# Performance work log

Measured on AMD Instinct MI355X. Metric: run time of the kernel, lower is better.

## Reference

```python
import jax, jax.numpy as jnp
import numpy as np

SEQ, BATCH, IN_DIM, HID = 1024, 512, 128, 128


def _linear_params(key, fan_in, fan_out):
    # matches torch nn.Linear default init: U(-1/sqrt(fan_in), 1/sqrt(fan_in))
    s = 1.0 / np.sqrt(fan_in)
    k1, k2 = jax.random.split(key)
    W = jax.random.uniform(k1, (fan_in, fan_out), minval=-s, maxval=s, dtype=jnp.float32)
    b = jax.random.uniform(k2, (fan_out,), minval=-s, maxval=s, dtype=jnp.float32)
    return W, b


def setup_inputs() -> dict:
    key = jax.random.key(0)
    ks = jax.random.split(key, 5)
    inputs = jax.random.normal(ks[0], (SEQ, BATCH, IN_DIM), dtype=jnp.float32)
    Wf, bf = _linear_params(ks[1], IN_DIM + HID, HID)
    Wi, bi = _linear_params(ks[2], IN_DIM + HID, HID)
    Wg, bg = _linear_params(ks[3], IN_DIM + HID, HID)
    Wo, bo = _linear_params(ks[4], IN_DIM + HID, HID)
    return {"inputs": inputs, "Wf": Wf, "bf": bf, "Wi": Wi, "bi": bi,
            "Wg": Wg, "bg": bg, "Wo": Wo, "bo": bo}


def reference(inputs, Wf, bf, Wi, bi, Wg, bg, Wo, bo):
    # inputs: [seq, batch, in_dim] (time-major, matches torch unbind(dim=0))
    B = inputs.shape[1]
    H = Wf.shape[1]
    h0 = jnp.zeros((B, H), dtype=inputs.dtype)
    c0 = jnp.zeros((B, H), dtype=inputs.dtype)

    def step(carry, x):
        hx, cx = carry
        comb = jnp.concatenate([x, hx], axis=1)  # [B, in_dim+H]
        f_lin = comb @ Wf + bf
        i_lin = comb @ Wi + bi
        g = jnp.tanh(comb @ Wg + bg)
        o = jax.nn.sigmoid(comb @ Wo + bo)
        # Quantum sampler, closed form:
        #  - RX(theta)|0> has <Z> = cos(theta)
        #  - CNOT chain over f-wires pulls Z_j back to Z_0...Z_j -> cumprod of cos
        #  - i-wires untouched by CNOTs -> plain cos
        #  probs = (<Z> + 1) / 2
        f = (jnp.cumprod(jnp.cos(f_lin), axis=1) + 1.0) * 0.5
        i = (jnp.cos(i_lin) + 1.0) * 0.5
        cx_new = f * cx + i * g
        hx_new = o * jnp.tanh(cx_new)
        return (hx_new, cx_new), hx_new

    (hx, cx), outputs = jax.lax.scan(step, (h0, c0), inputs)
    return outputs, hx, cx
```

## Files before the change

### kernel.cpp

```cpp
#include <hip/hip_runtime.h>

#define SEQ   1024
#define BATCH 512
#define HID   128

typedef __attribute__((ext_vector_type(8))) short          short8v;
typedef __attribute__((ext_vector_type(4))) float          float4v;
typedef __attribute__((ext_vector_type(4))) unsigned short ushort4v;

__device__ __forceinline__ unsigned short f2bf(float f) {
    union { float f; unsigned u; } v; v.f = f;
    return (unsigned short)((v.u + 0x7fffu + ((v.u >> 16) & 1u)) >> 16);
}
__device__ __forceinline__ float bf2f(unsigned short u) {
    union { unsigned u; float f; } v; v.u = ((unsigned)u) << 16;
    return v.f;
}
__device__ __forceinline__ unsigned packbf(float a, float b) {
    return (unsigned)f2bf(a) | ((unsigned)f2bf(b) << 16);
}
__device__ __forceinline__ float fast_cos(float x) {
    return __builtin_amdgcn_cosf(x * 0.15915494309189535f);
}
__device__ __forceinline__ float fast_sigmoid(float x) {
    return __builtin_amdgcn_rcpf(1.0f + __builtin_amdgcn_exp2f(-1.4426950408889634f * x));
}
__device__ __forceinline__ float fast_tanh(float x) {
    return 1.0f - 2.0f * __builtin_amdgcn_rcpf(1.0f + __builtin_amdgcn_exp2f(2.8853900817779268f * x));
}
template<int CTRL, int RM>
__device__ __forceinline__ float dpp1(float v) {
    union { float f; int i; } s, o, r;
    s.f = v; o.f = 1.0f;
    r.i = __builtin_amdgcn_update_dpp(o.i, s.i, CTRL, RM, 0xf, false);
    return r.f;
}
#define BAR() do { asm volatile("s_waitcnt lgkmcnt(0)" ::: "memory");  \
                   __builtin_amdgcn_s_barrier();                       \
                   __builtin_amdgcn_sched_barrier(0); } while (0)

__device__ __forceinline__ int zswz(int slot, int g, int c) {
    return slot * 512 + g * 128 + (c ^ ((c >> 5) << 4) ^ ((slot & 2) << 3));
}
__device__ __forceinline__ int gswz(int row, int g, int c) {
    return row * 512 + g * 128 + (c ^ ((c >> 5) << 4));
}

__global__ __launch_bounds__(512, 1) void qlstm_fused(
    const float* __restrict__ X,
    const float* __restrict__ Wf, const float* __restrict__ bfp,
    const float* __restrict__ Wi, const float* __restrict__ bip,
    const float* __restrict__ Wg, const float* __restrict__ bgp,
    const float* __restrict__ Wo, const float* __restrict__ bop,
    float* __restrict__ out)
{
    __shared__ short8v  wx_lds[8][4][4][64];
    __shared__ unsigned zr_lds[8 * 4 * 128];
    __shared__ float    ga_lds[2 * 4 * 128];
    __shared__ alignas(8)  unsigned short h_bf[2][HID];
    __shared__ alignas(16) unsigned short x_win[2][8][HID];
    __shared__ float scanT[2];

    const int tid = threadIdx.x, lane = tid & 63, wid = tid >> 6;
    const int l15 = lane & 15, kg = lane >> 4;
    const int b0 = blockIdx.x * 2;
    const int g  = wid >> 1;
    const int hb = wid & 1;
    const int cb = hb * 64;
    const float* Wsel = (g == 0) ? Wf : (g == 1) ? Wi : (g == 2) ? Wg : Wo;
    const float* bsel = (g == 0) ? bfp : (g == 1) ? bip : (g == 2) ? bgp : bop;

    #pragma unroll
    for (int n = 0; n < 4; ++n) {
        const int col = cb + n * 16 + l15;
        #pragma unroll
        for (int ks = 0; ks < 4; ++ks) {
            short8v wx;
            #pragma unroll
            for (int j = 0; j < 8; ++j)
                wx[j] = (short)f2bf(Wsel[(size_t)(ks * 32 + kg * 8 + j) * HID + col]);
            wx_lds[wid][n][ks][lane] = wx;
        }
    }
    BAR();

    short8v bwh[4][4];
    #pragma unroll
    for (int n = 0; n < 4; ++n) {
        const int col = cb + n * 16 + l15;
        #pragma unroll
        for (int ks = 0; ks < 4; ++ks) {
            short8v wh;
            #pragma unroll
            for (int j = 0; j < 8; ++j)
                wh[j] = (short)f2bf(Wsel[(size_t)(128 + ks * 32 + kg * 8 + j) * HID + col]);
            bwh[n][ks] = wh;
        }
    }
    float biasr[4];
    #pragma unroll
    for (int n = 0; n < 4; ++n) biasr[n] = bsel[cb + n * 16 + l15];

    if (tid < 128) ((unsigned*)h_bf)[tid] = 0u;

    const int crow = wid >> 1;
    const int ccol = (wid & 1) * 64 + lane;
    float c_reg = 0.f, h_last = 0.f;
    const int c_act = cb + lane;

    const int pt = tid - 256;
    const int sm = (pt >> 5) & 7;
    const int sc = pt & 31;
    const size_t xrow_off = ((size_t)(b0 + (sm & 1))) * HID + sc * 4;
    const int xw_boff = sm * 256 + ((((sc >> 1) ^ (sm & 7)) << 4) | ((sc & 1) << 3));

#define STAGE_XWIN(buf, s0) do {                                                    \
    const float* xp_ = X + ((size_t)((s0) + (sm >> 1)) * BATCH) * HID + xrow_off;   \
    float4v a_ = *(const float4v*)xp_;                                              \
    ushort4v o_;                                                                    \
    o_[0] = f2bf(a_[0]); o_[1] = f2bf(a_[1]); o_[2] = f2bf(a_[2]); o_[3] = f2bf(a_[3]); \
    *(ushort4v*)((char*)&x_win[buf][0][0] + xw_boff) = o_;                          \
} while (0)

#define XTILE(i, bn, buf) do {                                                      \
    float4v xa_;                                                                    \
    xa_[0] = biasr[i]; xa_[1] = biasr[i]; xa_[2] = biasr[i]; xa_[3] = biasr[i];     \
    _Pragma("unroll")                                                               \
    for (int ks_ = 0; ks_ < 4; ++ks_) {                                             \
        short8v axk = *(const short8v*)((const char*)&x_win[buf][0][0] +            \
            ((l15 & 7) * 256 + (((ks_ * 4 + kg) ^ (l15 & 7)) << 4)));               \
        xa_ = __builtin_amdgcn_mfma_f32_16x16x32_bf16(axk, wx_lds[wid][i][ks_][lane], xa_, 0, 0, 0); \
    }                                                                               \
    if (kg < 2) {                                                                   \
        const int cs_ = cb + (i) * 16 + l15;                                        \
        zr_lds[zswz(((bn) + kg * 2) & 7,     g, cs_)] = packbf(xa_[0], xa_[1]);     \
        zr_lds[zswz(((bn) + kg * 2 + 1) & 7, g, cs_)] = packbf(xa_[2], xa_[3]);     \
    }                                                                               \
} while (0)

    if (wid >= 4) { STAGE_XWIN(0, 0); STAGE_XWIN(1, 4); }
    BAR();
    XTILE(0, 0, 0);
    XTILE(1, 0, 0);
    XTILE(2, 0, 0);
    XTILE(3, 0, 0);
    BAR();

    float4v xg = {};

    #pragma unroll 1
    for (int t = 0; t < SEQ; ++t) {
        const int w = t & 3;
        const int W = t >> 2;
        const int bnext = (t & ~3) + 4;

        const unsigned zp = zr_lds[zswz(t & 7, g, c_act)];
        short8v ah[4];
        #pragma unroll
        for (int ks = 0; ks < 4; ++ks)
            ah[ks] = *(const short8v*)&h_bf[l15 & 1][ks * 32 + kg * 8];

        if (w == 0 && wid >= 4 && bnext + 4 < SEQ) {
            xg = *(const float4v*)(X + ((size_t)(bnext + 4 + (sm >> 1)) * BATCH) * HID + xrow_off);
        }

        float4v acc[4];
        #pragma unroll
        for (int n = 0; n < 4; ++n)
            #pragma unroll
            for (int j = 0; j < 4; ++j) acc[n][j] = 0.f;
        __builtin_amdgcn_s_setprio(1);
        #pragma unroll
        for (int ks = 0; ks < 4; ++ks)
            #pragma unroll
            for (int n = 0; n < 4; ++n)
                acc[n] = __builtin_amdgcn_mfma_f32_16x16x32_bf16(ah[ks], bwh[n][ks], acc[n], 0, 0, 0);
        __builtin_amdgcn_s_setprio(0);

        if (bnext < SEQ) {
            const int xbuf = (W + 1) & 1;
            switch (w) {
                case 0: XTILE(0, bnext, xbuf); break;
                case 1: XTILE(1, bnext, xbuf); break;
                case 2: XTILE(2, bnext, xbuf); break;
                default: XTILE(3, bnext, xbuf); break;
            }
        }

        float s0 = ((kg == 0) ? acc[0][0] : (kg == 1) ? acc[1][0]
                  : (kg == 2) ? acc[2][0] : acc[3][0]) + bf2f((unsigned short)(zp & 0xffffu));
        float s1 = ((kg == 0) ? acc[0][1] : (kg == 1) ? acc[1][1]
                  : (kg == 2) ? acc[2][1] : acc[3][1]) + bf2f((unsigned short)(zp >> 16));

        float v0, v1;
        if (g == 0) {
            float S0 = fast_cos(s0), S1 = fast_cos(s1);
            S0 *= dpp1<0x111, 0xf>(S0);  S1 *= dpp1<0x111, 0xf>(S1);
            S0 *= dpp1<0x112, 0xf>(S0);  S1 *= dpp1<0x112, 0xf>(S1);
            S0 *= dpp1<0x114, 0xf>(S0);  S1 *= dpp1<0x114, 0xf>(S1);
            S0 *= dpp1<0x118, 0xf>(S0);  S1 *= dpp1<0x118, 0xf>(S1);
            const float T00 = __shfl(S0, 15), T01 = __shfl(S0, 31), T02 = __shfl(S0, 47);
            const float T10 = __shfl(S1, 15), T11 = __shfl(S1, 31), T12 = __shfl(S1, 47);
            const float rp0 = (kg == 0) ? 1.f : (kg == 1) ? T00
                            : (kg == 2) ? T00 * T01 : T00 * T01 * T02;
            const float rp1 = (kg == 0) ? 1.f : (kg == 1) ? T10
                            : (kg == 2) ? T10 * T11 : T10 * T11 * T12;
            v0 = rp0 * S0;
            v1 = rp1 * S1;
            if (wid == 0 && lane == 63) { scanT[0] = v0; scanT[1] = v1; }
        } else if (g == 1) {
            v0 = (fast_cos(s0) + 1.f) * .5f;
            v1 = (fast_cos(s1) + 1.f) * .5f;
        } else if (g == 2) {
            v0 = fast_tanh(s0);
            v1 = fast_tanh(s1);
        } else {
            v0 = fast_sigmoid(s0);
            v1 = fast_sigmoid(s1);
        }
        ga_lds[gswz(0, g, c_act)] = v0;
        ga_lds[gswz(1, g, c_act)] = v1;

        BAR();

        if (wid < 4) {
            float fv = ga_lds[gswz(crow, 0, ccol)];
            if (wid & 1) fv *= scanT[crow];
            const float f  = (fv + 1.f) * 0.5f;
            const float iv = ga_lds[gswz(crow, 1, ccol)];
            const float gv = ga_lds[gswz(crow, 2, ccol)];
            const float ov = ga_lds[gswz(crow, 3, ccol)];
            const float cn = fmaf(f, c_reg, iv * gv);
            const float hn = ov * fast_tanh(cn);
            c_reg = cn; h_last = hn;
            h_bf[crow][ccol] = f2bf(hn);
            out[((size_t)t * BATCH + b0 + crow) * HID + ccol] = hn;
        } else if (w == 2 && bnext + 4 < SEQ) {
            ushort4v o_;
            o_[0] = f2bf(xg[0]); o_[1] = f2bf(xg[1]); o_[2] = f2bf(xg[2]); o_[3] = f2bf(xg[3]);
            *(ushort4v*)((char*)&x_win[W & 1][0][0] + xw_boff) = o_;
        }
        BAR();
    }

    if (wid < 4) {
        const size_t base = (size_t)SEQ * BATCH * HID;
        const size_t ro = (size_t)(b0 + crow) * HID + ccol;
        out[base + ro] = h_last;
        out[base + (size_t)BATCH * HID + ro] = c_reg;
    }
#undef STAGE_XWIN
#undef XTILE
}

extern "C" void kernel_launch(void* const* d_in, const int* in_sizes, int n_in,
                              void* d_out, int out_size, void* d_ws, size_t ws_size,
                              hipStream_t stream) {
    const float* X  = (const float*)d_in[0];
    const float* Wf = (const float*)d_in[1];
    const float* bf = (const float*)d_in[2];
    const float* Wi = (const float*)d_in[3];
    const float* bi = (const float*)d_in[4];
    const float* Wg = (const float*)d_in[5];
    const float* bg = (const float*)d_in[6];
    const float* Wo = (const float*)d_in[7];
    const float* bo = (const float*)d_in[8];
    float* out = (float*)d_out;
    (void)d_ws; (void)ws_size;

    qlstm_fused<<<BATCH / 2, 512, 0, stream>>>(
        X, Wf, bf, Wi, bi, Wg, bg, Wo, bo, out);
}
```

Baseline: 1.105 ms.

## Assign all four gates per column to each wave, removing gate-exchange LDS round trip

```diff
diff --git a/kernel.cpp b/kernel.cpp
--- a/kernel.cpp
+++ b/kernel.cpp
@@ -41,9 +41,6 @@
 
 __device__ __forceinline__ int zswz(int slot, int g, int c) {
     return slot * 512 + g * 128 + (c ^ ((c >> 5) << 4) ^ ((slot & 2) << 3));
-}
-__device__ __forceinline__ int gswz(int row, int g, int c) {
-    return row * 512 + g * 128 + (c ^ ((c >> 5) << 4));
 }
 
 __global__ __launch_bounds__(512, 1) void qlstm_fused(
@@ -56,57 +53,49 @@
 {
     __shared__ short8v  wx_lds[8][4][4][64];
     __shared__ unsigned zr_lds[8 * 4 * 128];
-    __shared__ float    ga_lds[2 * 4 * 128];
     __shared__ alignas(8)  unsigned short h_bf[2][HID];
     __shared__ alignas(16) unsigned short x_win[2][8][HID];
-    __shared__ float scanT[2];
+    __shared__ float scanW[8][2];
 
     const int tid = threadIdx.x, lane = tid & 63, wid = tid >> 6;
     const int l15 = lane & 15, kg = lane >> 4;
     const int b0 = blockIdx.x * 2;
-    const int g  = wid >> 1;
-    const int hb = wid & 1;
-    const int cb = hb * 64;
-    const float* Wsel = (g == 0) ? Wf : (g == 1) ? Wi : (g == 2) ? Wg : Wo;
-    const float* bsel = (g == 0) ? bfp : (g == 1) ? bip : (g == 2) ? bgp : bop;
+    const int col = wid * 16 + l15;
 
     #pragma unroll
-    for (int n = 0; n < 4; ++n) {
-        const int col = cb + n * 16 + l15;
+    for (int g2 = 0; g2 < 4; ++g2) {
+        const float* Wsel = (g2 == 0) ? Wf : (g2 == 1) ? Wi : (g2 == 2) ? Wg : Wo;
         #pragma unroll
         for (int ks = 0; ks < 4; ++ks) {
             short8v wx;
             #pragma unroll
             for (int j = 0; j < 8; ++j)
                 wx[j] = (short)f2bf(Wsel[(size_t)(ks * 32 + kg * 8 + j) * HID + col]);
-            wx_lds[wid][n][ks][lane] = wx;
+            wx_lds[wid][g2][ks][lane] = wx;
         }
     }
     BAR();
 
     short8v bwh[4][4];
+    float biasr[4];
     #pragma unroll
-    for (int n = 0; n < 4; ++n) {
-        const int col = cb + n * 16 + l15;
+    for (int g2 = 0; g2 < 4; ++g2) {
+        const float* Wsel = (g2 == 0) ? Wf : (g2 == 1) ? Wi : (g2 == 2) ? Wg : Wo;
+        const float* bsel = (g2 == 0) ? bfp : (g2 == 1) ? bip : (g2 == 2) ? bgp : bop;
         #pragma unroll
         for (int ks = 0; ks < 4; ++ks) {
             short8v wh;
             #pragma unroll
             for (int j = 0; j < 8; ++j)
                 wh[j] = (short)f2bf(Wsel[(size_t)(128 + ks * 32 + kg * 8 + j) * HID + col]);
-            bwh[n][ks] = wh;
-        }
-    }
-    float biasr[4];
-    #pragma unroll
-    for (int n = 0; n < 4; ++n) biasr[n] = bsel[cb + n * 16 + l15];
+            bwh[g2][ks] = wh;
+        }
+        biasr[g2] = bsel[col];
+    }
 
     if (tid < 128) ((unsigned*)h_bf)[tid] = 0u;
 
-    const int crow = wid >> 1;
-    const int ccol = (wid & 1) * 64 + lane;
-    float c_reg = 0.f, h_last = 0.f;
-    const int c_act = cb + lane;
+    float c_r0 = 0.f, c_r1 = 0.f, hL0 = 0.f, hL1 = 0.f;
 
     const int pt = tid - 256;
     const int sm = (pt >> 5) & 7;
@@ -122,19 +111,18 @@
     *(ushort4v*)((char*)&x_win[buf][0][0] + xw_boff) = o_;                          \
 } while (0)
 
-#define XTILE(i, bn, buf) do {                                                      \
+#define XTILE(G, bn, buf) do {                                                      \
     float4v xa_;                                                                    \
-    xa_[0] = biasr[i]; xa_[1] = biasr[i]; xa_[2] = biasr[i]; xa_[3] = biasr[i];     \
+    xa_[0] = biasr[G]; xa_[1] = biasr[G]; xa_[2] = biasr[G]; xa_[3] = biasr[G];     \
     _Pragma("unroll")                                                               \
     for (int ks_ = 0; ks_ < 4; ++ks_) {                                             \
         short8v axk = *(const short8v*)((const char*)&x_win[buf][0][0] +            \
             ((l15 & 7) * 256 + (((ks_ * 4 + kg) ^ (l15 & 7)) << 4)));               \
-        xa_ = __builtin_amdgcn_mfma_f32_16x16x32_bf16(axk, wx_lds[wid][i][ks_][lane], xa_, 0, 0, 0); \
+        xa_ = __builtin_amdgcn_mfma_f32_16x16x32_bf16(axk, wx_lds[wid][G][ks_][lane], xa_, 0, 0, 0); \
     }                                                                               \
     if (kg < 2) {                                                                   \
-        const int cs_ = cb + (i) * 16 + l15;                                        \
-        zr_lds[zswz(((bn) + kg * 2) & 7,     g, cs_)] = packbf(xa_[0], xa_[1]);     \
-        zr_lds[zswz(((bn) + kg * 2 + 1) & 7, g, cs_)] = packbf(xa_[2], xa_[3]);     \
+        zr_lds[zswz(((bn) + kg * 2) & 7,     G, col)] = packbf(xa_[0], xa_[1]);     \
+        zr_lds[zswz(((bn) + kg * 2 + 1) & 7, G, col)] = packbf(xa_[2], xa_[3]);     \
     }                                                                               \
 } while (0)
 
@@ -154,27 +142,29 @@
         const int W = t >> 2;
         const int bnext = (t & ~3) + 4;
 
-        const unsigned zp = zr_lds[zswz(t & 7, g, c_act)];
+        unsigned zp[4];
+        #pragma unroll
+        for (int g2 = 0; g2 < 4; ++g2)
+            zp[g2] = zr_lds[zswz(t & 7, g2, col)];
         short8v ah[4];
         #pragma unroll
         for (int ks = 0; ks < 4; ++ks)
             ah[ks] = *(const short8v*)&h_bf[l15 & 1][ks * 32 + kg * 8];
 
-        if (w == 0 && wid >= 4 && bnext + 4 < SEQ) {
+        if (w == 0 && wid >= 4 && bnext + 4 < SEQ)
             xg = *(const float4v*)(X + ((size_t)(bnext + 4 + (sm >> 1)) * BATCH) * HID + xrow_off);
-        }
 
         float4v acc[4];
         #pragma unroll
-        for (int n = 0; n < 4; ++n)
-            #pragma unroll
-            for (int j = 0; j < 4; ++j) acc[n][j] = 0.f;
+        for (int g2 = 0; g2 < 4; ++g2)
+            #pragma unroll
+            for (int j = 0; j < 4; ++j) acc[g2][j] = 0.f;
         __builtin_amdgcn_s_setprio(1);
         #pragma unroll
-        for (int ks = 0; ks < 4; ++ks)
-            #pragma unroll
-            for (int n = 0; n < 4; ++n)
-                acc[n] = __builtin_amdgcn_mfma_f32_16x16x32_bf16(ah[ks], bwh[n][ks], acc[n], 0, 0, 0);
+        for (int g2 = 0; g2 < 4; ++g2)
+            #pragma unroll
+            for (int ks = 0; ks < 4; ++ks)
+                acc[g2] = __builtin_amdgcn_mfma_f32_16x16x32_bf16(ah[ks], bwh[g2][ks], acc[g2], 0, 0, 0);
         __builtin_amdgcn_s_setprio(0);
 
         if (bnext < SEQ) {
@@ -187,55 +177,47 @@
             }
         }
 
-        float s0 = ((kg == 0) ? acc[0][0] : (kg == 1) ? acc[1][0]
-                  : (kg == 2) ? acc[2][0] : acc[3][0]) + bf2f((unsigned short)(zp & 0xffffu));
-        float s1 = ((kg == 0) ? acc[0][1] : (kg == 1) ? acc[1][1]
-                  : (kg == 2) ? acc[2][1] : acc[3][1]) + bf2f((unsigned short)(zp >> 16));
-
-        float v0, v1;
-        if (g == 0) {
-            float S0 = fast_cos(s0), S1 = fast_cos(s1);
-            S0 *= dpp1<0x111, 0xf>(S0);  S1 *= dpp1<0x111, 0xf>(S1);
-            S0 *= dpp1<0x112, 0xf>(S0);  S1 *= dpp1<0x112, 0xf>(S1);
-            S0 *= dpp1<0x114, 0xf>(S0);  S1 *= dpp1<0x114, 0xf>(S1);
-            S0 *= dpp1<0x118, 0xf>(S0);  S1 *= dpp1<0x118, 0xf>(S1);
-            const float T00 = __shfl(S0, 15), T01 = __shfl(S0, 31), T02 = __shfl(S0, 47);
-            const float T10 = __shfl(S1, 15), T11 = __shfl(S1, 31), T12 = __shfl(S1, 47);
-            const float rp0 = (kg == 0) ? 1.f : (kg == 1) ? T00
-                            : (kg == 2) ? T00 * T01 : T00 * T01 * T02;
-            const float rp1 = (kg == 0) ? 1.f : (kg == 1) ? T10
-                            : (kg == 2) ? T10 * T11 : T10 * T11 * T12;
-            v0 = rp0 * S0;
-            v1 = rp1 * S1;
-            if (wid == 0 && lane == 63) { scanT[0] = v0; scanT[1] = v1; }
-        } else if (g == 1) {
-            v0 = (fast_cos(s0) + 1.f) * .5f;
-            v1 = (fast_cos(s1) + 1.f) * .5f;
-        } else if (g == 2) {
-            v0 = fast_tanh(s0);
-            v1 = fast_tanh(s1);
-        } else {
-            v0 = fast_sigmoid(s0);
-            v1 = fast_sigmoid(s1);
-        }
-        ga_lds[gswz(0, g, c_act)] = v0;
-        ga_lds[gswz(1, g, c_act)] = v1;
+        const float fc0 = fast_cos(acc[0][0] + bf2f((unsigned short)(zp[0] & 0xffffu)));
+        const float fc1 = fast_cos(acc[0][1] + bf2f((unsigned short)(zp[0] >> 16)));
+        const float iv0 = (fast_cos(acc[1][0] + bf2f((unsigned short)(zp[1] & 0xffffu))) + 1.f) * 0.5f;
+        const float iv1 = (fast_cos(acc[1][1] + bf2f((unsigned short)(zp[1] >> 16))) + 1.f) * 0.5f;
+        const float gv0 = fast_tanh(acc[2][0] + bf2f((unsigned short)(zp[2] & 0xffffu)));
+        const float gv1 = fast_tanh(acc[2][1] + bf2f((unsigned short)(zp[2] >> 16)));
+        const float ov0 = fast_sigmoid(acc[3][0] + bf2f((unsigned short)(zp[3] & 0xffffu)));
+        const float ov1 = fast_sigmoid(acc[3][1] + bf2f((unsigned short)(zp[3] >> 16)));
+
+        float S0 = fc0, S1 = fc1;
+        S0 *= dpp1<0x111, 0xf>(S0);  S1 *= dpp1<0x111, 0xf>(S1);
+        S0 *= dpp1<0x112, 0xf>(S0);  S1 *= dpp1<0x112, 0xf>(S1);
+        S0 *= dpp1<0x114, 0xf>(S0);  S1 *= dpp1<0x114, 0xf>(S1);
+        S0 *= dpp1<0x118, 0xf>(S0);  S1 *= dpp1<0x118, 0xf>(S1);
+        if (lane == 15) { scanW[wid][0] = S0; scanW[wid][1] = S1; }
 
         BAR();
 
-        if (wid < 4) {
-            float fv = ga_lds[gswz(crow, 0, ccol)];
-            if (wid & 1) fv *= scanT[crow];
-            const float f  = (fv + 1.f) * 0.5f;
-            const float iv = ga_lds[gswz(crow, 1, ccol)];
-            const float gv = ga_lds[gswz(crow, 2, ccol)];
-            const float ov = ga_lds[gswz(crow, 3, ccol)];
-            const float cn = fmaf(f, c_reg, iv * gv);
-            const float hn = ov * fast_tanh(cn);
-            c_reg = cn; h_last = hn;
-            h_bf[crow][ccol] = f2bf(hn);
-            out[((size_t)t * BATCH + b0 + crow) * HID + ccol] = hn;
-        } else if (w == 2 && bnext + 4 < SEQ) {
+        float p0 = 1.f, p1 = 1.f;
+        #pragma unroll
+        for (int jw = 0; jw < 8; ++jw) {
+            const float a = scanW[jw][0], b = scanW[jw][1];
+            p0 *= (jw < wid) ? a : 1.f;
+            p1 *= (jw < wid) ? b : 1.f;
+        }
+        const float f0 = (p0 * S0 + 1.f) * 0.5f;
+        const float f1 = (p1 * S1 + 1.f) * 0.5f;
+
+        const float cn0 = fmaf(f0, c_r0, iv0 * gv0);
+        const float cn1 = fmaf(f1, c_r1, iv1 * gv1);
+        const float hn0 = ov0 * fast_tanh(cn0);
+        const float hn1 = ov1 * fast_tanh(cn1);
+        c_r0 = cn0; c_r1 = cn1; hL0 = hn0; hL1 = hn1;
+
+        if (kg == 0) {
+            h_bf[0][col] = f2bf(hn0);
+            h_bf[1][col] = f2bf(hn1);
+            out[((size_t)t * BATCH + b0) * HID + col] = hn0;
+            out[((size_t)t * BATCH + b0 + 1) * HID + col] = hn1;
+        }
+        if (wid >= 4 && w == 2 && bnext + 4 < SEQ) {
             ushort4v o_;
             o_[0] = f2bf(xg[0]); o_[1] = f2bf(xg[1]); o_[2] = f2bf(xg[2]); o_[3] = f2bf(xg[3]);
             *(ushort4v*)((char*)&x_win[W & 1][0][0] + xw_boff) = o_;
@@ -243,11 +225,12 @@
         BAR();
     }
 
-    if (wid < 4) {
+    if (kg == 0) {
         const size_t base = (size_t)SEQ * BATCH * HID;
-        const size_t ro = (size_t)(b0 + crow) * HID + ccol;
-        out[base + ro] = h_last;
-        out[base + (size_t)BATCH * HID + ro] = c_reg;
+        out[base + (size_t)b0 * HID + col]       = hL0;
+        out[base + (size_t)(b0 + 1) * HID + col] = hL1;
+        out[base + (size_t)BATCH * HID + (size_t)b0 * HID + col]       = c_r0;
+        out[base + (size_t)BATCH * HID + (size_t)(b0 + 1) * HID + col] = c_r1;
     }
 #undef STAGE_XWIN
 #undef XTILE
```

After: 1.227 ms. 1.11x slower.

## Move input-projection MFMAs to idle waves during elementwise phase

Applied to the files above, without the earlier changes.

```diff
diff --git a/kernel.cpp b/kernel.cpp
--- a/kernel.cpp
+++ b/kernel.cpp
@@ -57,6 +57,7 @@
     __shared__ short8v  wx_lds[8][4][4][64];
     __shared__ unsigned zr_lds[8 * 4 * 128];
     __shared__ float    ga_lds[2 * 4 * 128];
+    __shared__ float    bias_lds[4 * 128];
     __shared__ alignas(8)  unsigned short h_bf[2][HID];
     __shared__ alignas(16) unsigned short x_win[2][8][HID];
     __shared__ float scanT[2];
@@ -96,10 +97,8 @@
                 wh[j] = (short)f2bf(Wsel[(size_t)(128 + ks * 32 + kg * 8 + j) * HID + col]);
             bwh[n][ks] = wh;
         }
-    }
-    float biasr[4];
-    #pragma unroll
-    for (int n = 0; n < 4; ++n) biasr[n] = bsel[cb + n * 16 + l15];
+        if (kg == 0) bias_lds[g * 128 + col] = bsel[col];
+    }
 
     if (tid < 128) ((unsigned*)h_bf)[tid] = 0u;
 
@@ -122,28 +121,37 @@
     *(ushort4v*)((char*)&x_win[buf][0][0] + xw_boff) = o_;                          \
 } while (0)
 
-#define XTILE(i, bn, buf) do {                                                      \
-    float4v xa_;                                                                    \
-    xa_[0] = biasr[i]; xa_[1] = biasr[i]; xa_[2] = biasr[i]; xa_[3] = biasr[i];     \
+#define XT2(i, bn, buf) do {                                                        \
+    short8v axk[4];                                                                 \
     _Pragma("unroll")                                                               \
-    for (int ks_ = 0; ks_ < 4; ++ks_) {                                             \
-        short8v axk = *(const short8v*)((const char*)&x_win[buf][0][0] +            \
+    for (int ks_ = 0; ks_ < 4; ++ks_)                                               \
+        axk[ks_] = *(const short8v*)((const char*)&x_win[buf][0][0] +               \
             ((l15 & 7) * 256 + (((ks_ * 4 + kg) ^ (l15 & 7)) << 4)));               \
-        xa_ = __builtin_amdgcn_mfma_f32_16x16x32_bf16(axk, wx_lds[wid][i][ks_][lane], xa_, 0, 0, 0); \
-    }                                                                               \
-    if (kg < 2) {                                                                   \
-        const int cs_ = cb + (i) * 16 + l15;                                        \
-        zr_lds[zswz(((bn) + kg * 2) & 7,     g, cs_)] = packbf(xa_[0], xa_[1]);     \
-        zr_lds[zswz(((bn) + kg * 2 + 1) & 7, g, cs_)] = packbf(xa_[2], xa_[3]);     \
+    _Pragma("unroll")                                                               \
+    for (int uh_ = 0; uh_ < 2; ++uh_) {                                             \
+        const int u_  = (wid - 4) * 2 + uh_;                                        \
+        const int cs_ = uh_ * 64 + (i) * 16 + l15;                                  \
+        const float bb_ = bias_lds[(wid - 4) * 128 + cs_];                          \
+        float4v xa_; xa_[0] = bb_; xa_[1] = bb_; xa_[2] = bb_; xa_[3] = bb_;        \
+        _Pragma("unroll")                                                           \
+        for (int ks_ = 0; ks_ < 4; ++ks_)                                           \
+            xa_ = __builtin_amdgcn_mfma_f32_16x16x32_bf16(axk[ks_],                 \
+                      wx_lds[u_][i][ks_][lane], xa_, 0, 0, 0);                      \
+        if (kg < 2) {                                                               \
+            zr_lds[zswz(((bn) + kg * 2) & 7,     wid - 4, cs_)] = packbf(xa_[0], xa_[1]); \
+            zr_lds[zswz(((bn) + kg * 2 + 1) & 7, wid - 4, cs_)] = packbf(xa_[2], xa_[3]); \
+        }                                                                           \
     }                                                                               \
 } while (0)
 
     if (wid >= 4) { STAGE_XWIN(0, 0); STAGE_XWIN(1, 4); }
     BAR();
-    XTILE(0, 0, 0);
-    XTILE(1, 0, 0);
-    XTILE(2, 0, 0);
-    XTILE(3, 0, 0);
+    if (wid >= 4) {
+        XT2(0, 0, 0);
+        XT2(1, 0, 0);
+        XT2(2, 0, 0);
+        XT2(3, 0, 0);
+    }
     BAR();
 
     float4v xg = {};
@@ -160,9 +168,8 @@
         for (int ks = 0; ks < 4; ++ks)
             ah[ks] = *(const short8v*)&h_bf[l15 & 1][ks * 32 + kg * 8];
 
-        if (w == 0 && wid >= 4 && bnext + 4 < SEQ) {
+        if (w == 0 && wid >= 4 && bnext + 4 < SEQ)
             xg = *(const float4v*)(X + ((size_t)(bnext + 4 + (sm >> 1)) * BATCH) * HID + xrow_off);
-        }
 
         float4v acc[4];
         #pragma unroll
@@ -176,16 +183,6 @@
             for (int n = 0; n < 4; ++n)
                 acc[n] = __builtin_amdgcn_mfma_f32_16x16x32_bf16(ah[ks], bwh[n][ks], acc[n], 0, 0, 0);
         __builtin_amdgcn_s_setprio(0);
-
-        if (bnext < SEQ) {
-            const int xbuf = (W + 1) & 1;
-            switch (w) {
-                case 0: XTILE(0, bnext, xbuf); break;
-                case 1: XTILE(1, bnext, xbuf); break;
-                case 2: XTILE(2, bnext, xbuf); break;
-                default: XTILE(3, bnext, xbuf); break;
-            }
-        }
 
         float s0 = ((kg == 0) ? acc[0][0] : (kg == 1) ? acc[1][0]
                   : (kg == 2) ? acc[2][0] : acc[3][0]) + bf2f((unsigned short)(zp & 0xffffu));
@@ -235,10 +232,21 @@
             c_reg = cn; h_last = hn;
             h_bf[crow][ccol] = f2bf(hn);
             out[((size_t)t * BATCH + b0 + crow) * HID + ccol] = hn;
-        } else if (w == 2 && bnext + 4 < SEQ) {
-            ushort4v o_;
-            o_[0] = f2bf(xg[0]); o_[1] = f2bf(xg[1]); o_[2] = f2bf(xg[2]); o_[3] = f2bf(xg[3]);
-            *(ushort4v*)((char*)&x_win[W & 1][0][0] + xw_boff) = o_;
+        } else {
+            if (bnext < SEQ) {
+                const int xbuf = (W + 1) & 1;
+                switch (w) {
+                    case 0: XT2(0, bnext, xbuf); break;
+                    case 1: XT2(1, bnext, xbuf); break;
+                    case 2: XT2(2, bnext, xbuf); break;
+                    default: XT2(3, bnext, xbuf); break;
+                }
+            }
+            if (w == 2 && bnext + 4 < SEQ) {
+                ushort4v o_;
+                o_[0] = f2bf(xg[0]); o_[1] = f2bf(xg[1]); o_[2] = f2bf(xg[2]); o_[3] = f2bf(xg[3]);
+                *(ushort4v*)((char*)&x_win[W & 1][0][0] + xw_boff) = o_;
+            }
         }
         BAR();
     }
@@ -250,7 +258,7 @@
         out[base + (size_t)BATCH * HID + ro] = c_reg;
     }
 #undef STAGE_XWIN
-#undef XTILE
+#undef XT2
 }
 
 extern "C" void kernel_launch(void* const* d_in, const int* in_sizes, int n_in,
```

Measured after the change: 1.194 ms. 1.08x slower.

## Split block into recurrent and producer waves for input projection

Applied to the files above, without the earlier changes.

```diff
diff --git a/kernel.cpp b/kernel.cpp
--- a/kernel.cpp
+++ b/kernel.cpp
@@ -46,7 +46,7 @@
     return row * 512 + g * 128 + (c ^ ((c >> 5) << 4));
 }
 
-__global__ __launch_bounds__(512, 1) void qlstm_fused(
+__global__ __launch_bounds__(1024, 1) void qlstm_fused(
     const float* __restrict__ X,
     const float* __restrict__ Wf, const float* __restrict__ bfp,
     const float* __restrict__ Wi, const float* __restrict__ bip,
@@ -54,173 +54,172 @@
     const float* __restrict__ Wo, const float* __restrict__ bop,
     float* __restrict__ out)
 {
-    __shared__ short8v  wx_lds[8][4][4][64];
-    __shared__ unsigned zr_lds[8 * 4 * 128];
+    __shared__ unsigned zr_lds[16 * 4 * 128];
     __shared__ float    ga_lds[2 * 4 * 128];
     __shared__ alignas(8)  unsigned short h_bf[2][HID];
-    __shared__ alignas(16) unsigned short x_win[2][8][HID];
+    __shared__ alignas(16) unsigned short x_win[2][16][HID];
     __shared__ float scanT[2];
 
     const int tid = threadIdx.x, lane = tid & 63, wid = tid >> 6;
     const int l15 = lane & 15, kg = lane >> 4;
     const int b0 = blockIdx.x * 2;
-    const int g  = wid >> 1;
-    const int hb = wid & 1;
+    const bool prod = (wid >= 8);
+    const int rr = prod ? (wid - 8) : wid;
+    const int g  = rr >> 1;
+    const int hb = rr & 1;
     const int cb = hb * 64;
     const float* Wsel = (g == 0) ? Wf : (g == 1) ? Wi : (g == 2) ? Wg : Wo;
     const float* bsel = (g == 0) ? bfp : (g == 1) ? bip : (g == 2) ? bgp : bop;
 
-    #pragma unroll
-    for (int n = 0; n < 4; ++n) {
-        const int col = cb + n * 16 + l15;
+    short8v bw[4][4];
+    {
+        const int kbase = prod ? 0 : 128;
         #pragma unroll
-        for (int ks = 0; ks < 4; ++ks) {
-            short8v wx;
-            #pragma unroll
-            for (int j = 0; j < 8; ++j)
-                wx[j] = (short)f2bf(Wsel[(size_t)(ks * 32 + kg * 8 + j) * HID + col]);
-            wx_lds[wid][n][ks][lane] = wx;
-        }
-    }
-    BAR();
-
-    short8v bwh[4][4];
-    #pragma unroll
-    for (int n = 0; n < 4; ++n) {
-        const int col = cb + n * 16 + l15;
-        #pragma unroll
-        for (int ks = 0; ks < 4; ++ks) {
-            short8v wh;
-            #pragma unroll
-            for (int j = 0; j < 8; ++j)
-                wh[j] = (short)f2bf(Wsel[(size_t)(128 + ks * 32 + kg * 8 + j) * HID + col]);
-            bwh[n][ks] = wh;
+        for (int n = 0; n < 4; ++n) {
+            const int col = cb + n * 16 + l15;
+            #pragma unroll
+            for (int ks = 0; ks < 4; ++ks) {
+                const int k0 = kbase + ks * 32 + kg * 8;
+                short8v a;
+                #pragma unroll
+                for (int j = 0; j < 8; ++j)
+                    a[j] = (short)f2bf(Wsel[(size_t)(k0 + j) * HID + col]);
+                bw[n][ks] = a;
+            }
         }
     }
     float biasr[4];
     #pragma unroll
-    for (int n = 0; n < 4; ++n) biasr[n] = bsel[cb + n * 16 + l15];
+    for (int n = 0; n < 4; ++n) biasr[n] = prod ? bsel[cb + n * 16 + l15] : 0.f;
 
     if (tid < 128) ((unsigned*)h_bf)[tid] = 0u;
 
     const int crow = wid >> 1;
     const int ccol = (wid & 1) * 64 + lane;
+    const int c_act = cb + lane;
     float c_reg = 0.f, h_last = 0.f;
-    const int c_act = cb + lane;
-
-    const int pt = tid - 256;
-    const int sm = (pt >> 5) & 7;
-    const int sc = pt & 31;
+
+    const int pts = tid & 511;
+    const int sm  = pts >> 5;
+    const int sc  = pts & 31;
     const size_t xrow_off = ((size_t)(b0 + (sm & 1))) * HID + sc * 4;
-    const int xw_boff = sm * 256 + ((((sc >> 1) ^ (sm & 7)) << 4) | ((sc & 1) << 3));
-
-#define STAGE_XWIN(buf, s0) do {                                                    \
-    const float* xp_ = X + ((size_t)((s0) + (sm >> 1)) * BATCH) * HID + xrow_off;   \
+    const int xw8 = ((((sc >> 1) << 4) ^ ((sm & 7) << 4)) | ((sc & 1) << 3));
+    const int xsw = (l15 & 7) << 4;
+
+#define STAGE_XWIN(buf, s0v) do {                                                   \
+    const float* xp_ = X + ((size_t)((s0v) + (sm >> 1)) * BATCH) * HID + xrow_off;  \
     float4v a_ = *(const float4v*)xp_;                                              \
     ushort4v o_;                                                                    \
     o_[0] = f2bf(a_[0]); o_[1] = f2bf(a_[1]); o_[2] = f2bf(a_[2]); o_[3] = f2bf(a_[3]); \
-    *(ushort4v*)((char*)&x_win[buf][0][0] + xw_boff) = o_;                          \
+    *(ushort4v*)((char*)&x_win[buf][sm][0] + xw8) = o_;                             \
 } while (0)
 
-#define XTILE(i, bn, buf) do {                                                      \
+#define LOAD_AX(buf) do {                                                           \
+    const char* xb_ = (const char*)&x_win[buf][0][0] + l15 * 256;                   \
+    ax[0] = *(const short8v*)(xb_ + ((      kg * 16) ^ xsw));                       \
+    ax[1] = *(const short8v*)(xb_ + (( 64 + kg * 16) ^ xsw));                       \
+    ax[2] = *(const short8v*)(xb_ + ((128 + kg * 16) ^ xsw));                       \
+    ax[3] = *(const short8v*)(xb_ + ((192 + kg * 16) ^ xsw));                       \
+} while (0)
+
+#define XT(i, bn) do {                                                              \
     float4v xa_;                                                                    \
     xa_[0] = biasr[i]; xa_[1] = biasr[i]; xa_[2] = biasr[i]; xa_[3] = biasr[i];     \
-    _Pragma("unroll")                                                               \
-    for (int ks_ = 0; ks_ < 4; ++ks_) {                                             \
-        short8v axk = *(const short8v*)((const char*)&x_win[buf][0][0] +            \
-            ((l15 & 7) * 256 + (((ks_ * 4 + kg) ^ (l15 & 7)) << 4)));               \
-        xa_ = __builtin_amdgcn_mfma_f32_16x16x32_bf16(axk, wx_lds[wid][i][ks_][lane], xa_, 0, 0, 0); \
-    }                                                                               \
-    if (kg < 2) {                                                                   \
-        const int cs_ = cb + (i) * 16 + l15;                                        \
-        zr_lds[zswz(((bn) + kg * 2) & 7,     g, cs_)] = packbf(xa_[0], xa_[1]);     \
-        zr_lds[zswz(((bn) + kg * 2 + 1) & 7, g, cs_)] = packbf(xa_[2], xa_[3]);     \
-    }                                                                               \
+    xa_ = __builtin_amdgcn_mfma_f32_16x16x32_bf16(ax[0], bw[i][0], xa_, 0, 0, 0);   \
+    xa_ = __builtin_amdgcn_mfma_f32_16x16x32_bf16(ax[1], bw[i][1], xa_, 0, 0, 0);   \
+    xa_ = __builtin_amdgcn_mfma_f32_16x16x32_bf16(ax[2], bw[i][2], xa_, 0, 0, 0);   \
+    xa_ = __builtin_amdgcn_mfma_f32_16x16x32_bf16(ax[3], bw[i][3], xa_, 0, 0, 0);   \
+    const int se_ = ((bn) + kg * 2) & 15;                                           \
+    const int cs_ = cb + (i) * 16 + l15;                                            \
+    zr_lds[zswz(se_,     g, cs_)] = packbf(xa_[0], xa_[1]);                         \
+    zr_lds[zswz(se_ + 1, g, cs_)] = packbf(xa_[2], xa_[3]);                         \
 } while (0)
 
-    if (wid >= 4) { STAGE_XWIN(0, 0); STAGE_XWIN(1, 4); }
+    short8v ax[4] = {};
+    float4v xg = {};
+
+    if (prod) { STAGE_XWIN(0, 0); STAGE_XWIN(1, 8); }
     BAR();
-    XTILE(0, 0, 0);
-    XTILE(1, 0, 0);
-    XTILE(2, 0, 0);
-    XTILE(3, 0, 0);
+    if (prod) {
+        LOAD_AX(0);
+        XT(0, 0); XT(1, 0); XT(2, 0); XT(3, 0);
+    }
     BAR();
-
-    float4v xg = {};
 
     #pragma unroll 1
     for (int t = 0; t < SEQ; ++t) {
-        const int w = t & 3;
-        const int W = t >> 2;
-        const int bnext = (t & ~3) + 4;
-
-        const unsigned zp = zr_lds[zswz(t & 7, g, c_act)];
-        short8v ah[4];
-        #pragma unroll
-        for (int ks = 0; ks < 4; ++ks)
-            ah[ks] = *(const short8v*)&h_bf[l15 & 1][ks * 32 + kg * 8];
-
-        if (w == 0 && wid >= 4 && bnext + 4 < SEQ) {
-            xg = *(const float4v*)(X + ((size_t)(bnext + 4 + (sm >> 1)) * BATCH) * HID + xrow_off);
+        const int w = t & 7;
+        const int W = t >> 3;
+        const int bnext = (t & ~7) + 8;
+
+        if (!prod) {
+            const unsigned zp = zr_lds[zswz(t & 15, g, c_act)];
+            short8v ah[4];
+            #pragma unroll
+            for (int ks = 0; ks < 4; ++ks)
+                ah[ks] = *(const short8v*)&h_bf[l15 & 1][ks * 32 + kg * 8];
+
+            float4v acc[4];
+            #pragma unroll
+            for (int n = 0; n < 4; ++n)
+                #pragma unroll
+                for (int j = 0; j < 4; ++j) acc[n][j] = 0.f;
+            __builtin_amdgcn_s_setprio(1);
+            #pragma unroll
+            for (int ks = 0; ks < 4; ++ks)
+                #pragma unroll
+                for (int n = 0; n < 4; ++n)
+                    acc[n] = __builtin_amdgcn_mfma_f32_16x16x32_bf16(ah[ks], bw[n][ks], acc[n], 0, 0, 0);
+            __builtin_amdgcn_s_setprio(0);
+
+            float s0 = ((kg == 0) ? acc[0][0] : (kg == 1) ? acc[1][0]
+                      : (kg == 2) ? acc[2][0] : acc[3][0]) + bf2f((unsigned short)(zp & 0xffffu));
+            float s1 = ((kg == 0) ? acc[0][1] : (kg == 1) ? acc[1][1]
+                      : (kg == 2) ? acc[2][1] : acc[3][1]) + bf2f((unsigned short)(zp >> 16));
+
+            float v0, v1;
+            if (g == 0) {
+                float S0 = fast_cos(s0), S1 = fast_cos(s1);
+                S0 *= dpp1<0x111, 0xf>(S0);  S1 *= dpp1<0x111, 0xf>(S1);
+                S0 *= dpp1<0x112, 0xf>(S0);  S1 *= dpp1<0x112, 0xf>(S1);
+                S0 *= dpp1<0x114, 0xf>(S0);  S1 *= dpp1<0x114, 0xf>(S1);
+                S0 *= dpp1<0x118, 0xf>(S0);  S1 *= dpp1<0x118, 0xf>(S1);
+                const float T00 = __shfl(S0, 15), T01 = __shfl(S0, 31), T02 = __shfl(S0, 47);
+                const float T10 = __shfl(S1, 15), T11 = __shfl(S1, 31), T12 = __shfl(S1, 47);
+                const float rp0 = (kg == 0) ? 1.f : (kg == 1) ? T00
+                                : (kg == 2) ? T00 * T01 : T00 * T01 * T02;
+                const float rp1 = (kg == 0) ? 1.f : (kg == 1) ? T10
+                                : (kg == 2) ? T10 * T11 : T10 * T11 * T12;
+                v0 = rp0 * S0;
+                v1 = rp1 * S1;
+                if (wid == 0 && lane == 63) { scanT[0] = v0; scanT[1] = v1; }
+            } else if (g == 1) {
+                v0 = (fast_cos(s0) + 1.f) * .5f;
+                v1 = (fast_cos(s1) + 1.f) * .5f;
+            } else if (g == 2) {
+                v0 = fast_tanh(s0);
+                v1 = fast_tanh(s1);
+            } else {
+                v0 = fast_sigmoid(s0);
+                v1 = fast_sigmoid(s1);
+            }
+            ga_lds[gswz(0, g, c_act)] = v0;
+            ga_lds[gswz(1, g, c_act)] = v1;
+        } else {
+            if (w == 0) {
+                if (bnext < SEQ) LOAD_AX((W + 1) & 1);
+                if (bnext + 8 < SEQ)
+                    xg = *(const float4v*)(X + ((size_t)(bnext + 8 + (sm >> 1)) * BATCH) * HID + xrow_off);
+            }
+            if (bnext < SEQ && (w & 1) == hb) {
+                switch (w >> 1) {
+                    case 0: XT(0, bnext); break;
+                    case 1: XT(1, bnext); break;
+                    case 2: XT(2, bnext); break;
+                    default: XT(3, bnext); break;
+                }
+            }
         }
-
-        float4v acc[4];
-        #pragma unroll
-        for (int n = 0; n < 4; ++n)
-            #pragma unroll
-            for (int j = 0; j < 4; ++j) acc[n][j] = 0.f;
-        __builtin_amdgcn_s_setprio(1);
-        #pragma unroll
-        for (int ks = 0; ks < 4; ++ks)
-            #pragma unroll
-            for (int n = 0; n < 4; ++n)
-                acc[n] = __builtin_amdgcn_mfma_f32_16x16x32_bf16(ah[ks], bwh[n][ks], acc[n], 0, 0, 0);
-        __builtin_amdgcn_s_setprio(0);
-
-        if (bnext < SEQ) {
-            const int xbuf = (W + 1) & 1;
-            switch (w) {
-                case 0: XTILE(0, bnext, xbuf); break;
-                case 1: XTILE(1, bnext, xbuf); break;
-                case 2: XTILE(2, bnext, xbuf); break;
-                default: XTILE(3, bnext, xbuf); break;
-            }
-        }
-
-        float s0 = ((kg == 0) ? acc[0][0] : (kg == 1) ? acc[1][0]
-                  : (kg == 2) ? acc[2][0] : acc[3][0]) + bf2f((unsigned short)(zp & 0xffffu));
-        float s1 = ((kg == 0) ? acc[0][1] : (kg == 1) ? acc[1][1]
-                  : (kg == 2) ? acc[2][1] : acc[3][1]) + bf2f((unsigned short)(zp >> 16));
-
-        float v0, v1;
-        if (g == 0) {
-            float S0 = fast_cos(s0), S1 = fast_cos(s1);
-            S0 *= dpp1<0x111, 0xf>(S0);  S1 *= dpp1<0x111, 0xf>(S1);
-            S0 *= dpp1<0x112, 0xf>(S0);  S1 *= dpp1<0x112, 0xf>(S1);
-            S0 *= dpp1<0x114, 0xf>(S0);  S1 *= dpp1<0x114, 0xf>(S1);
-            S0 *= dpp1<0x118, 0xf>(S0);  S1 *= dpp1<0x118, 0xf>(S1);
-            const float T00 = __shfl(S0, 15), T01 = __shfl(S0, 31), T02 = __shfl(S0, 47);
-            const float T10 = __shfl(S1, 15), T11 = __shfl(S1, 31), T12 = __shfl(S1, 47);
-            const float rp0 = (kg == 0) ? 1.f : (kg == 1) ? T00
-                            : (kg == 2) ? T00 * T01 : T00 * T01 * T02;
-            const float rp1 = (kg == 0) ? 1.f : (kg == 1) ? T10
-                            : (kg == 2) ? T10 * T11 : T10 * T11 * T12;
-            v0 = rp0 * S0;
-            v1 = rp1 * S1;
-            if (wid == 0 && lane == 63) { scanT[0] = v0; scanT[1] = v1; }
-        } else if (g == 1) {
-            v0 = (fast_cos(s0) + 1.f) * .5f;
-            v1 = (fast_cos(s1) + 1.f) * .5f;
-        } else if (g == 2) {
-            v0 = fast_tanh(s0);
-            v1 = fast_tanh(s1);
-        } else {
-            v0 = fast_sigmoid(s0);
-            v1 = fast_sigmoid(s1);
-        }
-        ga_lds[gswz(0, g, c_act)] = v0;
-        ga_lds[gswz(1, g, c_act)] = v1;
-
         BAR();
 
         if (wid < 4) {
@@ -235,10 +234,10 @@
             c_reg = cn; h_last = hn;
             h_bf[crow][ccol] = f2bf(hn);
             out[((size_t)t * BATCH + b0 + crow) * HID + ccol] = hn;
-        } else if (w == 2 && bnext + 4 < SEQ) {
+        } else if (prod && w == 4 && bnext + 8 < SEQ) {
             ushort4v o_;
             o_[0] = f2bf(xg[0]); o_[1] = f2bf(xg[1]); o_[2] = f2bf(xg[2]); o_[3] = f2bf(xg[3]);
-            *(ushort4v*)((char*)&x_win[W & 1][0][0] + xw_boff) = o_;
+            *(ushort4v*)((char*)&x_win[W & 1][sm][0] + xw8) = o_;
         }
         BAR();
     }
@@ -250,7 +249,8 @@
         out[base + (size_t)BATCH * HID + ro] = c_reg;
     }
 #undef STAGE_XWIN
-#undef XTILE
+#undef LOAD_AX
+#undef XT
 }
 
 extern "C" void kernel_launch(void* const* d_in, const int* in_sizes, int n_in,
@@ -268,6 +268,6 @@
     float* out = (float*)d_out;
     (void)d_ws; (void)ws_size;
 
-    qlstm_fused<<<BATCH / 2, 512, 0, stream>>>(
+    qlstm_fused<<<BATCH / 2, 1024, 0, stream>>>(
         X, Wf, bf, Wi, bi, Wg, bg, Wo, bo, out);
 }
```

Measured after the change: 1.493 ms. 35.1% more time.
